# Kernel tuning notes

Hardware: AMD Instinct MI355X
Metric: run time of the kernel (lower is better)

## Reference

```python
import jax, jax.numpy as jnp
import numpy as np

RETURN_SHAPE = (128, 128)


def dht2(x):
    # Discrete Hartley Transform over the spatial axes (2, 3):
    # H = Re(FFT) - Im(FFT). Unnormalized, matching scipy.fft default.
    f = jnp.fft.fftn(x, axes=(2, 3))
    return f.real - f.imag


def setup_inputs() -> dict:
    key = jax.random.key(0)
    x = jax.random.normal(key, (8, 64, 256, 256), dtype=jnp.float32)
    return {"x": x}


def reference(x) -> jnp.ndarray:
    # Spectral pooling: DHT -> center crop in frequency domain -> DHT.
    h_out, w_out = RETURN_SHAPE
    H, W = x.shape[2], x.shape[3]
    d = dht2(x)
    sh = (H - h_out) // 2
    sw = (W - w_out) // 2
    cropped = d[:, :, sh:sh + h_out, sw:sw + w_out]
    return dht2(cropped).astype(jnp.float32)
```

## Files before the change

kernel.cpp:

```cpp
#include <hip/hip_runtime.h>
#include <math.h>


typedef __attribute__((ext_vector_type(8))) short bfrag;
typedef __attribute__((ext_vector_type(4))) float ffrag;

#define PI2_256 0.0245436926061702597f
#define PI2_128 0.0490873852123405194f

__device__ __forceinline__ unsigned short f2bf(float f) {
    union { float f; unsigned int u; } v; v.f = f;
    unsigned int r = v.u + 0x7fffu + ((v.u >> 16) & 1u);
    return (unsigned short)(r >> 16);
}

__device__ __forceinline__ bfrag pack8(float4 a, float4 b) {
    bfrag r;
    r[0] = (short)f2bf(a.x); r[1] = (short)f2bf(a.y);
    r[2] = (short)f2bf(a.z); r[3] = (short)f2bf(a.w);
    r[4] = (short)f2bf(b.x); r[5] = (short)f2bf(b.y);
    r[6] = (short)f2bf(b.z); r[7] = (short)f2bf(b.w);
    return r;
}

__device__ __forceinline__ uint2 packlohi(ffrag a) {
    uint2 r;
    r.x = (unsigned int)f2bf(a[0]) | ((unsigned int)f2bf(a[1]) << 16);
    r.y = (unsigned int)f2bf(a[2]) | ((unsigned int)f2bf(a[3]) << 16);
    return r;
}

template<int NCOLS, int K, int NTH>
__device__ __forceinline__ void stageB(const unsigned short* __restrict__ src,
                                       unsigned short* __restrict__ Lb, int t)
{
    constexpr int CHUNKS = NCOLS * K / 8;
#pragma unroll
    for (int i = 0; i < CHUNKS / NTH; ++i) {
        const int o = (t + i * NTH) * 8;
        const int j = o / K;
        const int k = o - j * K;
        const uint4 v = *(const uint4*)(src + o);
        *(uint4*)&Lb[j * K + (((k >> 3) ^ (j & 7)) << 3)] = v;
    }
}

template<int K>
__device__ __forceinline__ bfrag ldsB(const unsigned short* __restrict__ Lb, int j, int k)
{
    return *(const bfrag*)&Lb[j * K + (((k >> 3) ^ (j & 7)) << 3)];
}

__global__ __launch_bounds__(256) void gen_tables(unsigned short* __restrict__ ws)
{
    const int id = blockIdx.x * 256 + threadIdx.x;
    {
        const int j = id >> 8, m = id & 255;
        const int mult = (j < 128) ? (64 + j) : (320 - j);
        const int idx = (mult * m) & 255;
        float s, c; sincosf((float)idx * PI2_256, &s, &c);
        ws[id] = f2bf(c + s);
    }
    {
        const int u = id >> 9, k = id & 511;
        const int up = 64 + u;
        float s, c, val;
        if (k < 256) { sincosf((float)((up * k) & 255) * PI2_256, &s, &c); val = c; }
        else         { sincosf((float)((up * (k - 256)) & 255) * PI2_256, &s, &c); val = s; }
        ws[65536 + id] = f2bf(val);
    }
    if (id < 32768) {
        {
            const int j = id >> 7, m = id & 127;
            const int mult = (j < 128) ? j : (256 - j);
            const int idx = (mult * m) & 127;
            float s, c; sincosf((float)idx * PI2_128, &s, &c);
            ws[131072 + id] = f2bf(c + s);
        }
        {
            const int u = id >> 8, k = id & 255;
            float s, c, val;
            if (k < 128) { sincosf((float)((u * k) & 127) * PI2_128, &s, &c); val = c; }
            else         { sincosf((float)((u * (k - 128)) & 127) * PI2_128, &s, &c); val = s; }
            ws[163840 + id] = f2bf(val);
        }
    }
}

__global__ __launch_bounds__(256) void convertX(const float* __restrict__ X,
                                                unsigned short* __restrict__ Xb,
                                                int n8)
{
    const int stride = gridDim.x * 256;
    for (int i = blockIdx.x * 256 + threadIdx.x; i < n8; i += stride) {
        const float4 a = *(const float4*)(X + (size_t)i * 8);
        const float4 b = *(const float4*)(X + (size_t)i * 8 + 4);
        const bfrag v = pack8(a, b);
        *(uint4*)&Xb[(size_t)i * 8] = *(const uint4*)&v;
    }
}

__global__ __launch_bounds__(256, 2) void pass1(const unsigned short* __restrict__ Xb,
                                                const unsigned short* __restrict__ ws,
                                                unsigned short* __restrict__ Ct)
{
    __shared__ unsigned short Lb[64 * 256];

    const int t  = threadIdx.x;
    const int w  = t >> 6;
    const int ln = t & 15;
    const int q  = (t & 63) >> 4;
    const int img = blockIdx.x >> 2;
    const int h   = blockIdx.x & 3;

    stageB<64, 256, 256>(ws + h * 16384, Lb, t);
    __syncthreads();

    const unsigned short* __restrict__ Xi = Xb + (size_t)img * 65536;

    ffrag acc[4][4];
#pragma unroll
    for (int mt = 0; mt < 4; ++mt)
#pragma unroll
        for (int nt = 0; nt < 4; ++nt)
            acc[mt][nt] = (ffrag){0.f, 0.f, 0.f, 0.f};

#pragma unroll
    for (int kk = 0; kk < 8; ++kk) {
        const int k = kk * 32 + q * 8;
        bfrag A[4];
#pragma unroll
        for (int mt = 0; mt < 4; ++mt)
            A[mt] = *(const bfrag*)(Xi + (size_t)(64 * w + 16 * mt + ln) * 256 + k);
#pragma unroll
        for (int nt = 0; nt < 4; ++nt) {
            const bfrag B = ldsB<256>(Lb, nt * 16 + ln, k);
#pragma unroll
            for (int mt = 0; mt < 4; ++mt)
                acc[mt][nt] = __builtin_amdgcn_mfma_f32_16x16x32_bf16(A[mt], B, acc[mt][nt], 0, 0, 0);
        }
    }

    __syncthreads();
#pragma unroll
    for (int mt = 0; mt < 4; ++mt) {
#pragma unroll
        for (int nt = 0; nt < 4; ++nt) {
            const int cl = nt * 16 + ln;
            const int n2 = 16 * w + 4 * mt + q;
            const int phys = cl * 256 + (((n2 ^ ((cl & 7) << 3)) << 2));
            *(uint2*)&Lb[phys] = packlohi(acc[mt][nt]);
        }
    }
    __syncthreads();
    unsigned short* __restrict__ Co = Ct + (size_t)img * 65536 + 16384 * h;
#pragma unroll
    for (int j = 0; j < 8; ++j) {
        const int o   = (t + j * 256) * 8;
        const int row = o >> 8;
        const int ch  = (o & 255) >> 2;
        const int phys = row * 256 + (((ch ^ ((row & 7) << 3)) << 2));
        *(uint4*)&Co[o] = *(const uint4*)&Lb[phys];
    }
}

__global__ __launch_bounds__(256, 2) void pass2(const unsigned short* __restrict__ Ct,
                                                const unsigned short* __restrict__ ws,
                                                unsigned short* __restrict__ Dc)
{
    __shared__ unsigned short Lb[64 * 512];

    const int t  = threadIdx.x;
    const int w  = t >> 6;
    const int ln = t & 15;
    const int q  = (t & 63) >> 4;
    const int img = blockIdx.x >> 1;
    const int hu  = blockIdx.x & 1;

    stageB<64, 512, 256>(ws + 65536 + hu * 32768, Lb, t);
    __syncthreads();

    const unsigned short* __restrict__ Abase = Ct + (size_t)img * 65536;

    ffrag acc[2][4];
#pragma unroll
    for (int mt = 0; mt < 2; ++mt)
#pragma unroll
        for (int nt = 0; nt < 4; ++nt)
            acc[mt][nt] = (ffrag){0.f, 0.f, 0.f, 0.f};

#pragma unroll
    for (int kh = 0; kh < 2; ++kh) {
#pragma unroll
        for (int kk = 0; kk < 8; ++kk) {
            const int k = kk * 32 + q * 8;
            const int kfull = kh * 256 + k;
            bfrag A[2];
#pragma unroll
            for (int mt = 0; mt < 2; ++mt) {
                const int v = 32 * w + 16 * mt + ln;
                A[mt] = *(const bfrag*)(Abase + (size_t)(v + kh * 128) * 256 + k);
            }
#pragma unroll
            for (int nt = 0; nt < 4; ++nt) {
                const bfrag B = ldsB<512>(Lb, nt * 16 + ln, kfull);
#pragma unroll
                for (int mt = 0; mt < 2; ++mt)
                    acc[mt][nt] = __builtin_amdgcn_mfma_f32_16x16x32_bf16(A[mt], B, acc[mt][nt], 0, 0, 0);
            }
        }
    }
#pragma unroll
    for (int mt = 0; mt < 2; ++mt) {
        unsigned short* __restrict__ Do = Dc + (size_t)img * 16384 + 32 * w + 16 * mt + 4 * q;
#pragma unroll
        for (int nt = 0; nt < 4; ++nt) {
            *(uint2*)&Do[(size_t)(64 * hu + nt * 16 + ln) * 128] = packlohi(acc[mt][nt]);
        }
    }
}

__global__ __launch_bounds__(256, 2) void pass3(const unsigned short* __restrict__ Dc,
                                                const unsigned short* __restrict__ ws,
                                                unsigned short* __restrict__ C3t)
{
    __shared__ unsigned short Lb[128 * 128];

    const int t  = threadIdx.x;
    const int w  = t >> 6;
    const int ln = t & 15;
    const int q  = (t & 63) >> 4;
    const int img = blockIdx.x >> 1;
    const int hj  = blockIdx.x & 1;

    stageB<128, 128, 256>(ws + 131072 + hj * 16384, Lb, t);
    __syncthreads();

    const unsigned short* __restrict__ Abase = Dc + (size_t)img * 16384;

    ffrag acc[2][8];
#pragma unroll
    for (int mt = 0; mt < 2; ++mt)
#pragma unroll
        for (int nt = 0; nt < 8; ++nt)
            acc[mt][nt] = (ffrag){0.f, 0.f, 0.f, 0.f};

#pragma unroll
    for (int kk = 0; kk < 4; ++kk) {
        const int k = kk * 32 + q * 8;
        bfrag A[2];
#pragma unroll
        for (int mt = 0; mt < 2; ++mt) {
            const int p = 32 * w + 16 * mt + ln;
            A[mt] = *(const bfrag*)(Abase + (size_t)p * 128 + k);
        }
#pragma unroll
        for (int nt = 0; nt < 8; ++nt) {
            const bfrag B = ldsB<128>(Lb, nt * 16 + ln, k);
#pragma unroll
            for (int mt = 0; mt < 2; ++mt)
                acc[mt][nt] = __builtin_amdgcn_mfma_f32_16x16x32_bf16(A[mt], B, acc[mt][nt], 0, 0, 0);
        }
    }
#pragma unroll
    for (int mt = 0; mt < 2; ++mt) {
        unsigned short* __restrict__ Co = C3t + (size_t)img * 32768 + 32 * w + 16 * mt + 4 * q;
#pragma unroll
        for (int nt = 0; nt < 8; ++nt) {
            *(uint2*)&Co[(size_t)(128 * hj + nt * 16 + ln) * 128] = packlohi(acc[mt][nt]);
        }
    }
}

__global__ __launch_bounds__(256, 2) void pass4(const unsigned short* __restrict__ C3t,
                                                const unsigned short* __restrict__ ws,
                                                float* __restrict__ out)
{
    __shared__ unsigned short Lb[64 * 256];

    const int t  = threadIdx.x;
    const int w  = t >> 6;
    const int ln = t & 15;
    const int q  = (t & 63) >> 4;
    const int img = blockIdx.x >> 1;
    const int hu  = blockIdx.x & 1;

    stageB<64, 256, 256>(ws + 163840 + hu * 16384, Lb, t);
    __syncthreads();

    const unsigned short* __restrict__ Abase = C3t + (size_t)img * 32768;

    ffrag acc[2][4];
#pragma unroll
    for (int mt = 0; mt < 2; ++mt)
#pragma unroll
        for (int nt = 0; nt < 4; ++nt)
            acc[mt][nt] = (ffrag){0.f, 0.f, 0.f, 0.f};

#pragma unroll
    for (int kh = 0; kh < 2; ++kh) {
#pragma unroll
        for (int kk = 0; kk < 4; ++kk) {
            const int k = kk * 32 + q * 8;
            const int kfull = kh * 128 + k;
            bfrag A[2];
#pragma unroll
            for (int mt = 0; mt < 2; ++mt) {
                const int v = 32 * w + 16 * mt + ln;
                A[mt] = *(const bfrag*)(Abase + (size_t)(v + kh * 128) * 128 + k);
            }
#pragma unroll
            for (int nt = 0; nt < 4; ++nt) {
                const bfrag B = ldsB<256>(Lb, nt * 16 + ln, kfull);
#pragma unroll
                for (int mt = 0; mt < 2; ++mt)
                    acc[mt][nt] = __builtin_amdgcn_mfma_f32_16x16x32_bf16(A[mt], B, acc[mt][nt], 0, 0, 0);
            }
        }
    }
#pragma unroll
    for (int mt = 0; mt < 2; ++mt) {
        float* __restrict__ G = out + (size_t)img * 16384 + 32 * w + 16 * mt + 4 * q;
#pragma unroll
        for (int nt = 0; nt < 4; ++nt) {
            float4 o4 = make_float4(acc[mt][nt][0], acc[mt][nt][1], acc[mt][nt][2], acc[mt][nt][3]);
            *(float4*)&G[(size_t)(64 * hu + nt * 16 + ln) * 128] = o4;
        }
    }
}

__global__ __launch_bounds__(512, 2) void stage1_old(const float* __restrict__ X,
                                                     const unsigned short* __restrict__ ws,
                                                     float* __restrict__ dc)
{
    __shared__ unsigned short PQt[128 * 512];

    const int t  = threadIdx.x;
    const int w  = t >> 6;
    const int ln = t & 15;
    const int q  = (t & 63) >> 4;
    const int img = blockIdx.x;

    const float* __restrict__ Xi = X + (size_t)img * 65536;
    const unsigned short* __restrict__ W1 = ws;
    const unsigned short* __restrict__ W2 = ws + 65536;

    {
        ffrag acc[2][16];
#pragma unroll
        for (int mt = 0; mt < 2; ++mt)
#pragma unroll
            for (int nt = 0; nt < 16; ++nt)
                acc[mt][nt] = (ffrag){0.f, 0.f, 0.f, 0.f};

        const int rowA0 = 32 * w;
        for (int kk = 0; kk < 8; ++kk) {
            const int k = kk * 32 + q * 8;
            bfrag A[2];
#pragma unroll
            for (int mt = 0; mt < 2; ++mt) {
                const float* xp = Xi + (size_t)(rowA0 + 16 * mt + ln) * 256 + k;
                const float4 x0 = *(const float4*)xp;
                const float4 x1 = *(const float4*)(xp + 4);
                A[mt] = pack8(x0, x1);
            }
#pragma unroll
            for (int nt = 0; nt < 16; ++nt) {
                const int j = nt * 16 + ln;
                const bfrag B = *(const bfrag*)(W1 + j * 256 + k);
#pragma unroll
                for (int mt = 0; mt < 2; ++mt)
                    acc[mt][nt] = __builtin_amdgcn_mfma_f32_16x16x32_bf16(A[mt], B, acc[mt][nt], 0, 0, 0);
            }
        }
#pragma unroll
        for (int mt = 0; mt < 2; ++mt) {
#pragma unroll
            for (int nt = 0; nt < 16; ++nt) {
                const int c  = nt * 16 + ln;
                const int v  = c & 127;
                const int kb = ((c < 128) ? 0 : 256) + rowA0 + 16 * mt + 4 * q;
                const uint2 lohi = packlohi(acc[mt][nt]);
                const int phys = v * 512 + (((kb >> 3) ^ (v & 7)) << 3) + (kb & 7);
                *(uint2*)&PQt[phys] = lohi;
            }
        }
    }
    __syncthreads();

    {
        ffrag acc[8];
#pragma unroll
        for (int nt = 0; nt < 8; ++nt) acc[nt] = (ffrag){0.f, 0.f, 0.f, 0.f};

        const int u0 = 16 * w;
        for (int kk = 0; kk < 16; ++kk) {
            const int k = kk * 32 + q * 8;
            const bfrag A = *(const bfrag*)(W2 + (size_t)(u0 + ln) * 512 + k);
#pragma unroll
            for (int nt = 0; nt < 8; ++nt) {
                const int v = nt * 16 + ln;
                const int g = (k >> 3) ^ (v & 7);
                const bfrag B = *(const bfrag*)&PQt[v * 512 + (g << 3)];
                acc[nt] = __builtin_amdgcn_mfma_f32_16x16x32_bf16(A, B, acc[nt], 0, 0, 0);
            }
        }
        float* __restrict__ D = dc + (size_t)img * 16384;
#pragma unroll
        for (int nt = 0; nt < 8; ++nt) {
#pragma unroll
            for (int r = 0; r < 4; ++r) {
                const int u = u0 + 4 * q + r;
                const int v = nt * 16 + ln;
                D[u * 128 + v] = acc[nt][r];
            }
        }
    }
}

__global__ __launch_bounds__(256, 2) void stage2_old(const unsigned short* __restrict__ ws,
                                                     float* __restrict__ io)
{
    __shared__ unsigned short Dcb[128 * 128];
    __shared__ unsigned short PQ2[64 * 256];

    const int t  = threadIdx.x;
    const int w  = t >> 6;
    const int ln = t & 15;
    const int q  = (t & 63) >> 4;
    const int img = blockIdx.x;

    float* __restrict__ G = io + (size_t)img * 16384;
    const unsigned short* __restrict__ W3 = ws + 131072;
    const unsigned short* __restrict__ W4 = ws + 163840;

    {
        const int p = t >> 1, half = t & 1;
        const float* src = G + p * 128 + half * 64;
#pragma unroll
        for (int g = 0; g < 8; ++g) {
            const float4 a = *(const float4*)(src + g * 8);
            const float4 b = *(const float4*)(src + g * 8 + 4);
            const int m0 = half * 64 + g * 8;
            const int gran = (m0 >> 3) ^ (p & 7);
            uint4 val;
            val.x = (unsigned int)f2bf(a.x) | ((unsigned int)f2bf(a.y) << 16);
            val.y = (unsigned int)f2bf(a.z) | ((unsigned int)f2bf(a.w) << 16);
            val.z = (unsigned int)f2bf(b.x) | ((unsigned int)f2bf(b.y) << 16);
            val.w = (unsigned int)f2bf(b.z) | ((unsigned int)f2bf(b.w) << 16);
            *(uint4*)&Dcb[p * 128 + gran * 8] = val;
        }
    }
    __syncthreads();

    for (int vh = 0; vh < 2; ++vh) {
        ffrag acc[2][8];
#pragma unroll
        for (int mt = 0; mt < 2; ++mt)
#pragma unroll
            for (int nt = 0; nt < 8; ++nt)
                acc[mt][nt] = (ffrag){0.f, 0.f, 0.f, 0.f};

        const int p0 = 32 * w;
        for (int kk = 0; kk < 4; ++kk) {
            const int k = kk * 32 + q * 8;
            bfrag A[2];
#pragma unroll
            for (int mt = 0; mt < 2; ++mt) {
                const int p = p0 + 16 * mt + ln;
                const int g = (k >> 3) ^ (p & 7);
                A[mt] = *(const bfrag*)&Dcb[p * 128 + g * 8];
            }
#pragma unroll
            for (int nt = 0; nt < 8; ++nt) {
                const int c = nt * 16 + ln;
                const int j = (c < 64) ? (64 * vh + c) : (128 + 64 * vh + (c - 64));
                const bfrag B = *(const bfrag*)(W3 + j * 128 + k);
#pragma unroll
                for (int mt = 0; mt < 2; ++mt)
                    acc[mt][nt] = __builtin_amdgcn_mfma_f32_16x16x32_bf16(A[mt], B, acc[mt][nt], 0, 0, 0);
            }
        }
        __syncthreads();
#pragma unroll
        for (int mt = 0; mt < 2; ++mt) {
#pragma unroll
            for (int nt = 0; nt < 8; ++nt) {
                const int c  = nt * 16 + ln;
                const int v  = c & 63;
                const int kb = ((c < 64) ? 0 : 128) + p0 + 16 * mt + 4 * q;
                const uint2 lohi = packlohi(acc[mt][nt]);
                const int phys = v * 256 + (((kb >> 3) ^ (v & 7)) << 3) + (kb & 7);
                *(uint2*)&PQ2[phys] = lohi;
            }
        }
        __syncthreads();

        ffrag o[2][4];
#pragma unroll
        for (int mt = 0; mt < 2; ++mt)
#pragma unroll
            for (int nt = 0; nt < 4; ++nt)
                o[mt][nt] = (ffrag){0.f, 0.f, 0.f, 0.f};

        const int u0 = 32 * w;
        for (int kk = 0; kk < 8; ++kk) {
            const int k = kk * 32 + q * 8;
            bfrag A[2];
#pragma unroll
            for (int mt = 0; mt < 2; ++mt)
                A[mt] = *(const bfrag*)(W4 + (size_t)(u0 + 16 * mt + ln) * 256 + k);
#pragma unroll
            for (int nt = 0; nt < 4; ++nt) {
                const int v = nt * 16 + ln;
                const int g = (k >> 3) ^ (v & 7);
                const bfrag B = *(const bfrag*)&PQ2[v * 256 + (g << 3)];
#pragma unroll
                for (int mt = 0; mt < 2; ++mt)
                    o[mt][nt] = __builtin_amdgcn_mfma_f32_16x16x32_bf16(A[mt], B, o[mt][nt], 0, 0, 0);
            }
        }
#pragma unroll
        for (int mt = 0; mt < 2; ++mt) {
#pragma unroll
            for (int nt = 0; nt < 4; ++nt) {
#pragma unroll
                for (int r = 0; r < 4; ++r) {
                    const int u = u0 + 16 * mt + 4 * q + r;
                    const int v = 64 * vh + nt * 16 + ln;
                    G[u * 128 + v] = o[mt][nt][r];
                }
            }
        }
    }
}

extern "C" void kernel_launch(void* const* d_in, const int* in_sizes, int n_in,
                              void* d_out, int out_size, void* d_ws, size_t ws_size,
                              hipStream_t stream)
{
    const float* x = (const float*)d_in[0];
    float* out = (float*)d_out;
    unsigned short* tw = (unsigned short*)d_ws;

    gen_tables<<<dim3(256), dim3(256), 0, stream>>>(tw);

    int G = 512;
    while (G > 1 && (size_t)262144 * (size_t)G + 393216 > ws_size) G >>= 1;

    if ((size_t)262144 * (size_t)G + 393216 <= ws_size) {
        unsigned short* regA = tw + 196608;
        unsigned short* regB = regA + (size_t)G * 65536;
        const int nchunks = 512 / G;
        for (int ci = 0; ci < nchunks; ++ci) {
            const float* xc = x + (size_t)ci * G * 65536;
            float* oc = out + (size_t)ci * G * 16384;
            convertX<<<dim3(2048), dim3(256), 0, stream>>>(xc, regB, G * 8192);
            pass1<<<dim3(4 * G), dim3(256), 0, stream>>>(regB, tw, regA);
            pass2<<<dim3(2 * G), dim3(256), 0, stream>>>(regA, tw, regB);
            pass3<<<dim3(2 * G), dim3(256), 0, stream>>>(regB, tw, regA);
            pass4<<<dim3(2 * G), dim3(256), 0, stream>>>(regA, tw, oc);
        }
    } else {
        stage1_old<<<dim3(512), dim3(512), 0, stream>>>(x, tw, out);
        stage2_old<<<dim3(512), dim3(256), 0, stream>>>(tw, out);
    }
}
```

Measured before the change: 323.0 us.

## Fuse fp32-to-bf16 conversion into pass1 and merge pass3/pass4 into one kernel

Drops the separate convertX kernel, so pass1 now reads fp32 input directly and packs it to bf16 in registers. It also replaces pass3 and pass4 with one per-image kernel that keeps the cropped spectrum and the intermediate product in swizzled LDS instead of round-tripping through global memory. The goal is fewer launches and less HBM traffic for intermediates. In exchange, pass1 reads twice the bytes per A fragment, the fused kernel runs one block per image with twiddles read from global rather than LDS, and its final output uses scalar, less coalesced stores.

```diff
diff --git a/kernel.cpp b/kernel.cpp
--- a/kernel.cpp
+++ b/kernel.cpp
@@ -87,20 +87,7 @@
     }
 }
 
-__global__ __launch_bounds__(256) void convertX(const float* __restrict__ X,
-                                                unsigned short* __restrict__ Xb,
-                                                int n8)
-{
-    const int stride = gridDim.x * 256;
-    for (int i = blockIdx.x * 256 + threadIdx.x; i < n8; i += stride) {
-        const float4 a = *(const float4*)(X + (size_t)i * 8);
-        const float4 b = *(const float4*)(X + (size_t)i * 8 + 4);
-        const bfrag v = pack8(a, b);
-        *(uint4*)&Xb[(size_t)i * 8] = *(const uint4*)&v;
-    }
-}
-
-__global__ __launch_bounds__(256, 2) void pass1(const unsigned short* __restrict__ Xb,
+__global__ __launch_bounds__(256, 2) void pass1(const float* __restrict__ X,
                                                 const unsigned short* __restrict__ ws,
                                                 unsigned short* __restrict__ Ct)
 {
@@ -116,7 +103,7 @@
     stageB<64, 256, 256>(ws + h * 16384, Lb, t);
     __syncthreads();
 
-    const unsigned short* __restrict__ Xi = Xb + (size_t)img * 65536;
+    const float* __restrict__ Xi = X + (size_t)img * 65536;
 
     ffrag acc[4][4];
 #pragma unroll
@@ -130,8 +117,12 @@
         const int k = kk * 32 + q * 8;
         bfrag A[4];
 #pragma unroll
-        for (int mt = 0; mt < 4; ++mt)
-            A[mt] = *(const bfrag*)(Xi + (size_t)(64 * w + 16 * mt + ln) * 256 + k);
+        for (int mt = 0; mt < 4; ++mt) {
+            const float* xp = Xi + (size_t)(64 * w + 16 * mt + ln) * 256 + k;
+            const float4 x0 = *(const float4*)xp;
+            const float4 x1 = *(const float4*)(xp + 4);
+            A[mt] = pack8(x0, x1);
+        }
 #pragma unroll
         for (int nt = 0; nt < 4; ++nt) {
             const bfrag B = ldsB<256>(Lb, nt * 16 + ln, k);
@@ -220,111 +211,114 @@
     }
 }
 
-__global__ __launch_bounds__(256, 2) void pass3(const unsigned short* __restrict__ Dc,
-                                                const unsigned short* __restrict__ ws,
-                                                unsigned short* __restrict__ C3t)
-{
-    __shared__ unsigned short Lb[128 * 128];
+__global__ __launch_bounds__(256, 2) void stage2f(const unsigned short* __restrict__ Dc,
+                                                  const unsigned short* __restrict__ ws,
+                                                  float* __restrict__ out)
+{
+    __shared__ unsigned short Dcb[128 * 128];
+    __shared__ unsigned short PQ2[64 * 256];
 
     const int t  = threadIdx.x;
     const int w  = t >> 6;
     const int ln = t & 15;
     const int q  = (t & 63) >> 4;
-    const int img = blockIdx.x >> 1;
-    const int hj  = blockIdx.x & 1;
-
-    stageB<128, 128, 256>(ws + 131072 + hj * 16384, Lb, t);
-    __syncthreads();
-
-    const unsigned short* __restrict__ Abase = Dc + (size_t)img * 16384;
-
-    ffrag acc[2][8];
-#pragma unroll
-    for (int mt = 0; mt < 2; ++mt)
-#pragma unroll
-        for (int nt = 0; nt < 8; ++nt)
-            acc[mt][nt] = (ffrag){0.f, 0.f, 0.f, 0.f};
-
-#pragma unroll
-    for (int kk = 0; kk < 4; ++kk) {
-        const int k = kk * 32 + q * 8;
-        bfrag A[2];
-#pragma unroll
-        for (int mt = 0; mt < 2; ++mt) {
-            const int p = 32 * w + 16 * mt + ln;
-            A[mt] = *(const bfrag*)(Abase + (size_t)p * 128 + k);
-        }
-#pragma unroll
-        for (int nt = 0; nt < 8; ++nt) {
-            const bfrag B = ldsB<128>(Lb, nt * 16 + ln, k);
-#pragma unroll
-            for (int mt = 0; mt < 2; ++mt)
-                acc[mt][nt] = __builtin_amdgcn_mfma_f32_16x16x32_bf16(A[mt], B, acc[mt][nt], 0, 0, 0);
-        }
-    }
-#pragma unroll
-    for (int mt = 0; mt < 2; ++mt) {
-        unsigned short* __restrict__ Co = C3t + (size_t)img * 32768 + 32 * w + 16 * mt + 4 * q;
-#pragma unroll
-        for (int nt = 0; nt < 8; ++nt) {
-            *(uint2*)&Co[(size_t)(128 * hj + nt * 16 + ln) * 128] = packlohi(acc[mt][nt]);
-        }
-    }
-}
-
-__global__ __launch_bounds__(256, 2) void pass4(const unsigned short* __restrict__ C3t,
-                                                const unsigned short* __restrict__ ws,
-                                                float* __restrict__ out)
-{
-    __shared__ unsigned short Lb[64 * 256];
-
-    const int t  = threadIdx.x;
-    const int w  = t >> 6;
-    const int ln = t & 15;
-    const int q  = (t & 63) >> 4;
-    const int img = blockIdx.x >> 1;
-    const int hu  = blockIdx.x & 1;
-
-    stageB<64, 256, 256>(ws + 163840 + hu * 16384, Lb, t);
-    __syncthreads();
-
-    const unsigned short* __restrict__ Abase = C3t + (size_t)img * 32768;
-
-    ffrag acc[2][4];
-#pragma unroll
-    for (int mt = 0; mt < 2; ++mt)
-#pragma unroll
-        for (int nt = 0; nt < 4; ++nt)
-            acc[mt][nt] = (ffrag){0.f, 0.f, 0.f, 0.f};
-
-#pragma unroll
-    for (int kh = 0; kh < 2; ++kh) {
-#pragma unroll
+    const int img = blockIdx.x;
+
+    float* __restrict__ G = out + (size_t)img * 16384;
+    const unsigned short* __restrict__ W3 = ws + 131072;
+    const unsigned short* __restrict__ W4 = ws + 163840;
+
+    {
+        const unsigned short* __restrict__ src = Dc + (size_t)img * 16384;
+#pragma unroll
+        for (int j = 0; j < 8; ++j) {
+            const int o  = (t + j * 256) * 8;
+            const int p  = o >> 7;
+            const int m0 = o & 127;
+            const int gran = (m0 >> 3) ^ (p & 7);
+            *(uint4*)&Dcb[p * 128 + gran * 8] = *(const uint4*)(src + o);
+        }
+    }
+    __syncthreads();
+
+    for (int vh = 0; vh < 2; ++vh) {
+        ffrag acc[2][8];
+#pragma unroll
+        for (int mt = 0; mt < 2; ++mt)
+#pragma unroll
+            for (int nt = 0; nt < 8; ++nt)
+                acc[mt][nt] = (ffrag){0.f, 0.f, 0.f, 0.f};
+
+        const int p0 = 32 * w;
         for (int kk = 0; kk < 4; ++kk) {
             const int k = kk * 32 + q * 8;
-            const int kfull = kh * 128 + k;
             bfrag A[2];
 #pragma unroll
             for (int mt = 0; mt < 2; ++mt) {
-                const int v = 32 * w + 16 * mt + ln;
-                A[mt] = *(const bfrag*)(Abase + (size_t)(v + kh * 128) * 128 + k);
-            }
-#pragma unroll
-            for (int nt = 0; nt < 4; ++nt) {
-                const bfrag B = ldsB<256>(Lb, nt * 16 + ln, kfull);
+                const int p = p0 + 16 * mt + ln;
+                const int g = (k >> 3) ^ (p & 7);
+                A[mt] = *(const bfrag*)&Dcb[p * 128 + g * 8];
+            }
+#pragma unroll
+            for (int nt = 0; nt < 8; ++nt) {
+                const int c = nt * 16 + ln;
+                const int j = (c < 64) ? (64 * vh + c) : (128 + 64 * vh + (c - 64));
+                const bfrag B = *(const bfrag*)(W3 + j * 128 + k);
 #pragma unroll
                 for (int mt = 0; mt < 2; ++mt)
                     acc[mt][nt] = __builtin_amdgcn_mfma_f32_16x16x32_bf16(A[mt], B, acc[mt][nt], 0, 0, 0);
             }
         }
-    }
-#pragma unroll
-    for (int mt = 0; mt < 2; ++mt) {
-        float* __restrict__ G = out + (size_t)img * 16384 + 32 * w + 16 * mt + 4 * q;
-#pragma unroll
-        for (int nt = 0; nt < 4; ++nt) {
-            float4 o4 = make_float4(acc[mt][nt][0], acc[mt][nt][1], acc[mt][nt][2], acc[mt][nt][3]);
-            *(float4*)&G[(size_t)(64 * hu + nt * 16 + ln) * 128] = o4;
+        __syncthreads();
+#pragma unroll
+        for (int mt = 0; mt < 2; ++mt) {
+#pragma unroll
+            for (int nt = 0; nt < 8; ++nt) {
+                const int c  = nt * 16 + ln;
+                const int v  = c & 63;
+                const int kb = ((c < 64) ? 0 : 128) + p0 + 16 * mt + 4 * q;
+                const uint2 lohi = packlohi(acc[mt][nt]);
+                const int phys = v * 256 + (((kb >> 3) ^ (v & 7)) << 3) + (kb & 7);
+                *(uint2*)&PQ2[phys] = lohi;
+            }
+        }
+        __syncthreads();
+
+        ffrag o2[2][4];
+#pragma unroll
+        for (int mt = 0; mt < 2; ++mt)
+#pragma unroll
+            for (int nt = 0; nt < 4; ++nt)
+                o2[mt][nt] = (ffrag){0.f, 0.f, 0.f, 0.f};
+
+        const int u0 = 32 * w;
+        for (int kk = 0; kk < 8; ++kk) {
+            const int k = kk * 32 + q * 8;
+            bfrag A[2];
+#pragma unroll
+            for (int mt = 0; mt < 2; ++mt)
+                A[mt] = *(const bfrag*)(W4 + (size_t)(u0 + 16 * mt + ln) * 256 + k);
+#pragma unroll
+            for (int nt = 0; nt < 4; ++nt) {
+                const int v = nt * 16 + ln;
+                const int g = (k >> 3) ^ (v & 7);
+                const bfrag B = *(const bfrag*)&PQ2[v * 256 + (g << 3)];
+#pragma unroll
+                for (int mt = 0; mt < 2; ++mt)
+                    o2[mt][nt] = __builtin_amdgcn_mfma_f32_16x16x32_bf16(A[mt], B, o2[mt][nt], 0, 0, 0);
+            }
+        }
+#pragma unroll
+        for (int mt = 0; mt < 2; ++mt) {
+#pragma unroll
+            for (int nt = 0; nt < 4; ++nt) {
+#pragma unroll
+                for (int r = 0; r < 4; ++r) {
+                    const int u = u0 + 16 * mt + 4 * q + r;
+                    const int v = 64 * vh + nt * 16 + ln;
+                    G[u * 128 + v] = o2[mt][nt][r];
+                }
+            }
         }
     }
 }
@@ -546,20 +540,18 @@
     gen_tables<<<dim3(256), dim3(256), 0, stream>>>(tw);
 
     int G = 512;
-    while (G > 1 && (size_t)262144 * (size_t)G + 393216 > ws_size) G >>= 1;
-
-    if ((size_t)262144 * (size_t)G + 393216 <= ws_size) {
+    while (G > 1 && (size_t)163840 * (size_t)G + 393216 > ws_size) G >>= 1;
+
+    if ((size_t)163840 * (size_t)G + 393216 <= ws_size) {
         unsigned short* regA = tw + 196608;
         unsigned short* regB = regA + (size_t)G * 65536;
         const int nchunks = 512 / G;
         for (int ci = 0; ci < nchunks; ++ci) {
             const float* xc = x + (size_t)ci * G * 65536;
             float* oc = out + (size_t)ci * G * 16384;
-            convertX<<<dim3(2048), dim3(256), 0, stream>>>(xc, regB, G * 8192);
-            pass1<<<dim3(4 * G), dim3(256), 0, stream>>>(regB, tw, regA);
+            pass1<<<dim3(4 * G), dim3(256), 0, stream>>>(xc, tw, regA);
             pass2<<<dim3(2 * G), dim3(256), 0, stream>>>(regA, tw, regB);
-            pass3<<<dim3(2 * G), dim3(256), 0, stream>>>(regB, tw, regA);
-            pass4<<<dim3(2 * G), dim3(256), 0, stream>>>(regA, tw, oc);
+            stage2f<<<dim3(G), dim3(256), 0, stream>>>(regB, tw, oc);
         }
     } else {
         stage1_old<<<dim3(512), dim3(512), 0, stream>>>(x, tw, out);
```

Result: faster. 291.6 us (-9.7%).
